# Kernel tuning notes

Hardware: AMD Instinct MI355X
Metric: run time of the kernel (lower is better)

## Reference

```python
import jax, jax.numpy as jnp
import numpy as np

N_NODES = 50000
N_EDGES = 1600000
IN_CH = 128
HID_CH = 128


def setup_inputs() -> dict:
    key = jax.random.key(0)
    ks = jax.random.split(key, 8)
    node_embed = jax.random.normal(ks[0], (N_NODES, IN_CH), dtype=jnp.float32)
    node_pos = jax.random.normal(ks[1], (N_NODES, 3), dtype=jnp.float32)
    edge_index = jax.random.randint(ks[2], (2, N_EDGES), 0, N_NODES, dtype=jnp.int64)
    # Linear weights stored as [in, out] so y = x @ W + b (matches torch x @ W.T + b)
    W_res = jax.random.normal(ks[3], (IN_CH, HID_CH), dtype=jnp.float32) / np.sqrt(IN_CH)
    W_msg = jax.random.normal(ks[4], (2 * IN_CH + 1, HID_CH), dtype=jnp.float32) / np.sqrt(2 * IN_CH + 1)
    b_msg = jax.random.normal(ks[5], (HID_CH,), dtype=jnp.float32) * 0.01
    W_upd = jax.random.normal(ks[6], (IN_CH + HID_CH, HID_CH), dtype=jnp.float32) / np.sqrt(IN_CH + HID_CH)
    b_upd = jax.random.normal(ks[7], (HID_CH,), dtype=jnp.float32) * 0.01
    return {"node_embed": node_embed, "node_pos": node_pos, "edge_index": edge_index,
            "W_res": W_res, "W_msg": W_msg, "b_msg": b_msg, "W_upd": W_upd, "b_upd": b_upd}


def reference(node_embed, node_pos, edge_index, W_res, W_msg, b_msg, W_upd, b_upd):
    row, col = edge_index[0], edge_index[1]
    # squared distance per edge: [E, 1]
    diff = node_pos[row] - node_pos[col]
    dist = jnp.sum(diff * diff, axis=1, keepdims=True)
    # message MLP on concat(src, tgt, dist): [E, 2*in+1] -> [E, hidden]
    msg_in = jnp.concatenate([node_embed[row], node_embed[col], dist], axis=-1)
    msg = jax.nn.relu(msg_in @ W_msg + b_msg)
    # scatter-sum messages into target nodes (index = col, as in original)
    aggr = jax.ops.segment_sum(msg, col, num_segments=N_NODES)
    upd_in = jnp.concatenate([node_embed, aggr], axis=-1)
    new_node_embed = node_embed @ W_res + jax.nn.relu(upd_in @ W_upd + b_upd)
    return new_node_embed
```

## Files before the change

### kernel.cpp

```cpp
#include <hip/hip_runtime.h>
#include <hip/hip_bf16.h>
#include <cstdint>


typedef __bf16 bf16x8 __attribute__((ext_vector_type(8)));
typedef float floatx4 __attribute__((ext_vector_type(4)));
typedef float floatx2 __attribute__((ext_vector_type(2)));
typedef unsigned int uintx4 __attribute__((ext_vector_type(4)));

#define BUCKET_CAP 128
#define NBINS 256
#define BIN_CAP 10240
#define PASS2_SPLIT 4
#define CUR_STRIDE 32

__device__ __forceinline__ ushort f2bf(float f) {
  union { float f; uint i; } v; v.f = f;
  uint r = v.i + 0x7fff + ((v.i >> 16) & 1);
  return (ushort)(r >> 16);
}
__device__ __forceinline__ bf16x8 load_frag(const ushort* p) {
  uint4 v = *(const uint4*)p;
  return __builtin_bit_cast(bf16x8, v);
}
__device__ __forceinline__ floatx2 pmax0(floatx2 a) {
#if __has_builtin(__builtin_elementwise_max)
  return __builtin_elementwise_max(a, (floatx2)(0.f));
#else
  floatx2 r; r.x = fmaxf(a.x, 0.f); r.y = fmaxf(a.y, 0.f); return r;
#endif
}
__device__ __forceinline__ floatx2 cvtpk2(uint qu) {
#if __has_builtin(__builtin_amdgcn_cvt_pk_f32_fp8)
  return __builtin_amdgcn_cvt_pk_f32_fp8((int)qu, false);
#else
  floatx2 o = {__builtin_amdgcn_cvt_f32_fp8((int)qu, 0),
               __builtin_amdgcn_cvt_f32_fp8((int)qu, 1)};
  return o;
#endif
}

struct WSrc { const float* s[5]; };

__global__ __launch_bounds__(256) void k01_cast_bin(
    const float* __restrict__ embed, ushort* __restrict__ Eb, int n4, int nb_cast,
    WSrc ws, ushort* __restrict__ Wt,
    const int* __restrict__ ei, int E,
    uint* __restrict__ bin_cursor, uint* __restrict__ binned, int bb)
{
  __shared__ uint hist[NBINS];
  __shared__ uint sbase[NBINS];
  __shared__ uint lcur[NBINS];

  if ((int)blockIdx.x >= bb) {
    int cb = blockIdx.x - bb;
    if (cb < nb_cast) {
      int i = cb * 256 + threadIdx.x;
      if (i < n4) {
        float4 v = ((const float4*)embed)[i];
        ushort4 o;
        o.x = f2bf(v.x); o.y = f2bf(v.y); o.z = f2bf(v.z); o.w = f2bf(v.w);
        ((ushort4*)Eb)[i] = o;
      }
      return;
    }
    int wb = cb - nb_cast;
    const float* s = ws.s[wb];
    ushort* d = Wt + wb * 16384;
    for (int i = threadIdx.x; i < 16384; i += 256) {
      int k = i >> 7, n = i & 127;
      d[n * 128 + k] = f2bf(s[i]);
    }
    return;
  }

  const int t = threadIdx.x;
  hist[t] = 0;
  __syncthreads();

  const int e0 = blockIdx.x * 2048 + t * 8;
  int rr[8], cc[8];
  bool any = (e0 < E);
  if (any) {
    int4 r0 = ((const int4*)(ei + e0))[0];
    int4 r1 = ((const int4*)(ei + e0))[1];
    int4 c0 = ((const int4*)(ei + E + e0))[0];
    int4 c1 = ((const int4*)(ei + E + e0))[1];
    rr[0]=r0.x; rr[1]=r0.y; rr[2]=r0.z; rr[3]=r0.w;
    rr[4]=r1.x; rr[5]=r1.y; rr[6]=r1.z; rr[7]=r1.w;
    cc[0]=c0.x; cc[1]=c0.y; cc[2]=c0.z; cc[3]=c0.w;
    cc[4]=c1.x; cc[5]=c1.y; cc[6]=c1.z; cc[7]=c1.w;
#pragma unroll
    for (int j = 0; j < 8; ++j) {
      if (e0 + j < E) atomicAdd(&hist[cc[j] >> 8], 1u);
    }
  }
  __syncthreads();
  uint h = hist[t];
  sbase[t] = h ? atomicAdd(bin_cursor + t * CUR_STRIDE, h) : 0u;
  lcur[t] = 0;
  __syncthreads();
  if (any) {
#pragma unroll
    for (int j = 0; j < 8; ++j) {
      if (e0 + j < E) {
        int b = cc[j] >> 8;
        uint ofs = atomicAdd(&lcur[b], 1u);
        uint idx = sbase[b] + ofs;
        if (idx < BIN_CAP)
          binned[(size_t)b * BIN_CAP + idx] = ((uint)cc[j] << 16) | (uint)rr[j];
      }
    }
  }
}

__global__ __launch_bounds__(256) void k2_proj_pass2(
    const ushort* __restrict__ Ab, int M, int rt,
    const ushort* __restrict__ W1t, const ushort* __restrict__ W2t,
    const float* __restrict__ b_msg, const float* __restrict__ pos,
    unsigned char* __restrict__ P1, ushort* __restrict__ P2b,
    const uint* __restrict__ bin_cursor, const uint* __restrict__ binned,
    int* __restrict__ counts, uint* __restrict__ recs)
{
  if ((int)blockIdx.x >= rt) {
    int b = blockIdx.x - rt;
    int bin = b / PASS2_SPLIT, part = b % PASS2_SPLIT;
    int cnt = (int)min(bin_cursor[bin * CUR_STRIDE], (uint)BIN_CAP);
    int s0 = (int)((long)cnt * part / PASS2_SPLIT);
    int s1 = (int)((long)cnt * (part + 1) / PASS2_SPLIT);
    const uint* src = binned + (size_t)bin * BIN_CAP;

    int i = s0 + threadIdx.x;
    for (; i + 768 < s1; i += 1024) {
      uint rc[4];
      rc[0] = src[i]; rc[1] = src[i + 256]; rc[2] = src[i + 512]; rc[3] = src[i + 768];
      float d[4];
#pragma unroll
      for (int j = 0; j < 4; ++j) {
        uint r = rc[j] & 0xffffu, c = rc[j] >> 16;
        float dx = pos[3 * r + 0] - pos[3 * c + 0];
        float dy = pos[3 * r + 1] - pos[3 * c + 1];
        float dz = pos[3 * r + 2] - pos[3 * c + 2];
        d[j] = dx * dx + dy * dy + dz * dz;
      }
#pragma unroll
      for (int j = 0; j < 4; ++j) {
        uint c = rc[j] >> 16;
        int slot = atomicAdd(counts + c, 1);
        if (slot < BUCKET_CAP)
          recs[(size_t)c * BUCKET_CAP + slot] = (rc[j] << 16) | (uint)f2bf(d[j]);
      }
    }
    for (; i < s1; i += 256) {
      uint rc = src[i];
      uint r = rc & 0xffffu, c = rc >> 16;
      float dx = pos[3 * r + 0] - pos[3 * c + 0];
      float dy = pos[3 * r + 1] - pos[3 * c + 1];
      float dz = pos[3 * r + 2] - pos[3 * c + 2];
      float dist = dx * dx + dy * dy + dz * dz;
      int slot = atomicAdd(counts + c, 1);
      if (slot < BUCKET_CAP)
        recs[(size_t)c * BUCKET_CAP + slot] = (rc << 16) | (uint)f2bf(dist);
    }
    return;
  }

  const int wv = threadIdx.x >> 6, lane = threadIdx.x & 63;
  const int q = lane >> 4, lr = lane & 15;
  const int m0 = blockIdx.x * 32;
  const int n0 = wv * 32;

  const ushort* Wt2[2] = {W1t, W2t};
  bf16x8 bfr[2][2][4];
#pragma unroll
  for (int ws = 0; ws < 2; ++ws)
#pragma unroll
    for (int nt = 0; nt < 2; ++nt) {
      int colc = n0 + nt * 16 + lr;
#pragma unroll
      for (int kc = 0; kc < 4; ++kc)
        bfr[ws][nt][kc] = load_frag(Wt2[ws] + colc * 128 + kc * 32 + q * 8);
    }

  floatx4 z = {0.f, 0.f, 0.f, 0.f};
  floatx4 acc[2][2][2];
#pragma unroll
  for (int ws = 0; ws < 2; ++ws)
#pragma unroll
    for (int mt = 0; mt < 2; ++mt)
#pragma unroll
      for (int nt = 0; nt < 2; ++nt) acc[ws][mt][nt] = z;

  const int r0 = min(m0 + lr, M - 1);
  const int r1 = min(m0 + 16 + lr, M - 1);
#pragma unroll
  for (int kc = 0; kc < 4; ++kc) {
    bf16x8 a0 = load_frag(Ab + (size_t)r0 * 128 + kc * 32 + q * 8);
    bf16x8 a1 = load_frag(Ab + (size_t)r1 * 128 + kc * 32 + q * 8);
#pragma unroll
    for (int ws = 0; ws < 2; ++ws)
#pragma unroll
      for (int nt = 0; nt < 2; ++nt) {
        acc[ws][0][nt] = __builtin_amdgcn_mfma_f32_16x16x32_bf16(a0, bfr[ws][nt][kc], acc[ws][0][nt], 0, 0, 0);
        acc[ws][1][nt] = __builtin_amdgcn_mfma_f32_16x16x32_bf16(a1, bfr[ws][nt][kc], acc[ws][1][nt], 0, 0, 0);
      }
  }

#pragma unroll
  for (int nt = 0; nt < 2; ++nt) {
    int colc = n0 + nt * 16 + lr;
    float bias = b_msg[colc];
#pragma unroll
    for (int mt = 0; mt < 2; ++mt)
#pragma unroll
      for (int i = 0; i < 4; ++i) {
        int r = m0 + mt * 16 + q * 4 + i;
        if (r < M) {
          int p8 = __builtin_amdgcn_cvt_pk_fp8_f32(acc[0][mt][nt][i], 0.f, 0, false);
          P1[(size_t)r * 128 + colc] = (unsigned char)(p8 & 0xff);
          P2b[(size_t)r * 128 + colc] = f2bf(acc[1][mt][nt][i] + bias);
        }
      }
  }
}

__global__ __launch_bounds__(256) void aggregate(const int* __restrict__ counts,
                                                 const uint* __restrict__ recs,
                                                 const unsigned char* __restrict__ P1,
                                                 const ushort* __restrict__ P2b,
                                                 const float* __restrict__ wd,
                                                 ushort* __restrict__ aggr, int M)
{
  const int lane = threadIdx.x & 63;
  const int ch = lane * 2;
  const int wid = blockIdx.x * 4 + (threadIdx.x >> 6);
  const int nw = gridDim.x * 4;

  float2 wl = *(const float2*)(wd + ch);
  floatx2 wv = {wl.x, wl.y};

  for (int n = wid; n < M; n += nw) {
    uint p2u = *(const uint*)(P2b + (size_t)n * 128 + ch);
    floatx2 p2 = {__int_as_float((int)(p2u << 16)),
                  __int_as_float((int)(p2u & 0xffff0000u))};

    const int cnt = min(counts[n], BUCKET_CAP);
    const uint* base = recs + (size_t)n * BUCKET_CAP;

    floatx2 accA = {0.f, 0.f}, accB = {0.f, 0.f};

    auto edge = [&](uint rec, floatx2& acc) {
      float d = __int_as_float((int)(rec << 16));
      uint off = ((rec >> 9) & 0x007fff80u) | (uint)ch;
      uint qu = (uint)*(const ushort*)(P1 + off);
#if __has_builtin(__builtin_elementwise_fma)
      floatx2 u = __builtin_elementwise_fma((floatx2)(d), wv, p2);
#else
      floatx2 u = (floatx2)(d) * wv + p2;
#endif
      floatx2 t = cvtpk2(qu) + u;
      acc += pmax0(t);
    };

    int i = 0;
    for (; i + 8 <= cnt; i += 8) {
      uintx4 ra = __builtin_nontemporal_load((const uintx4*)(base + i));
      uintx4 rb = __builtin_nontemporal_load((const uintx4*)(base + i + 4));
      edge(ra.x, accA); edge(ra.y, accB); edge(ra.z, accA); edge(ra.w, accB);
      edge(rb.x, accA); edge(rb.y, accB); edge(rb.z, accA); edge(rb.w, accB);
    }
    for (; i < cnt; ++i) edge(base[i], accA);

    floatx2 acc = accA + accB;
    uint o = (uint)f2bf(acc.x) | ((uint)f2bf(acc.y) << 16);
    *(uint*)(aggr + (size_t)n * 128 + ch) = o;
  }
}

__global__ __launch_bounds__(256) void gemm_upd_mfma(
    const ushort* __restrict__ Eb, const ushort* __restrict__ Gb, int M,
    const ushort* __restrict__ Wu1t, const ushort* __restrict__ Wu2t,
    const ushort* __restrict__ Wrt, const float* __restrict__ b_upd,
    float* __restrict__ out)
{
  const int wv = threadIdx.x >> 6, lane = threadIdx.x & 63;
  const int q = lane >> 4, lr = lane & 15;
  const int m0 = blockIdx.x * 32;
  const int n0 = wv * 32;

  bf16x8 b1[2][4], b2[2][4], br[2][4];
#pragma unroll
  for (int nt = 0; nt < 2; ++nt) {
    int colc = n0 + nt * 16 + lr;
#pragma unroll
    for (int kc = 0; kc < 4; ++kc) {
      b1[nt][kc] = load_frag(Wu1t + colc * 128 + kc * 32 + q * 8);
      b2[nt][kc] = load_frag(Wu2t + colc * 128 + kc * 32 + q * 8);
      br[nt][kc] = load_frag(Wrt  + colc * 128 + kc * 32 + q * 8);
    }
  }

  floatx4 z = {0.f, 0.f, 0.f, 0.f};
  floatx4 acc_u[2][2], acc_r[2][2];
#pragma unroll
  for (int mt = 0; mt < 2; ++mt)
#pragma unroll
    for (int nt = 0; nt < 2; ++nt) { acc_u[mt][nt] = z; acc_r[mt][nt] = z; }

  const int r0 = min(m0 + lr, M - 1);
  const int r1 = min(m0 + 16 + lr, M - 1);
#pragma unroll
  for (int kc = 0; kc < 4; ++kc) {
    bf16x8 ae0 = load_frag(Eb + (size_t)r0 * 128 + kc * 32 + q * 8);
    bf16x8 ae1 = load_frag(Eb + (size_t)r1 * 128 + kc * 32 + q * 8);
    bf16x8 ag0 = load_frag(Gb + (size_t)r0 * 128 + kc * 32 + q * 8);
    bf16x8 ag1 = load_frag(Gb + (size_t)r1 * 128 + kc * 32 + q * 8);
#pragma unroll
    for (int nt = 0; nt < 2; ++nt) {
      acc_u[0][nt] = __builtin_amdgcn_mfma_f32_16x16x32_bf16(ae0, b1[nt][kc], acc_u[0][nt], 0, 0, 0);
      acc_u[1][nt] = __builtin_amdgcn_mfma_f32_16x16x32_bf16(ae1, b1[nt][kc], acc_u[1][nt], 0, 0, 0);
      acc_u[0][nt] = __builtin_amdgcn_mfma_f32_16x16x32_bf16(ag0, b2[nt][kc], acc_u[0][nt], 0, 0, 0);
      acc_u[1][nt] = __builtin_amdgcn_mfma_f32_16x16x32_bf16(ag1, b2[nt][kc], acc_u[1][nt], 0, 0, 0);
      acc_r[0][nt] = __builtin_amdgcn_mfma_f32_16x16x32_bf16(ae0, br[nt][kc], acc_r[0][nt], 0, 0, 0);
      acc_r[1][nt] = __builtin_amdgcn_mfma_f32_16x16x32_bf16(ae1, br[nt][kc], acc_r[1][nt], 0, 0, 0);
    }
  }

#pragma unroll
  for (int nt = 0; nt < 2; ++nt) {
    int colc = n0 + nt * 16 + lr;
    float bias = b_upd[colc];
#pragma unroll
    for (int mt = 0; mt < 2; ++mt)
#pragma unroll
      for (int i = 0; i < 4; ++i) {
        int r = m0 + mt * 16 + q * 4 + i;
        if (r < M)
          out[(size_t)r * 128 + colc] = acc_r[mt][nt][i] + fmaxf(acc_u[mt][nt][i] + bias, 0.f);
      }
  }
}

extern "C" void kernel_launch(void* const* d_in, const int* in_sizes, int n_in,
                              void* d_out, int out_size, void* d_ws, size_t ws_size,
                              hipStream_t stream)
{
  const float* embed = (const float*)d_in[0];
  const float* pos   = (const float*)d_in[1];
  const int*   ei    = (const int*)d_in[2];
  const float* W_res = (const float*)d_in[3];
  const float* W_msg = (const float*)d_in[4];
  const float* b_msg = (const float*)d_in[5];
  const float* W_upd = (const float*)d_in[6];
  const float* b_upd = (const float*)d_in[7];
  float* out = (float*)d_out;

  const int M = in_sizes[0] / 128;
  const int E = in_sizes[2] / 2;

  ushort* Eb = (ushort*)d_ws;
  unsigned char* P1f8 = (unsigned char*)(Eb + (size_t)M * 128);
  ushort* P2b = (ushort*)(P1f8 + (size_t)M * 128);
  ushort* Gb  = P2b + (size_t)M * 128;
  ushort* Wt  = Gb  + (size_t)M * 128;
  uint*   recs = (uint*)(Wt + 5 * 16384);
  uint*   binned = (uint*)(recs + (size_t)M * BUCKET_CAP);
  int*    counts = (int*)(binned + (size_t)NBINS * BIN_CAP);
  uint*   bin_cursor = (uint*)(counts + M);

  (void)hipMemsetAsync(counts, 0, (size_t)(M + NBINS * CUR_STRIDE) * sizeof(int), stream);

  WSrc wsrc;
  wsrc.s[0] = W_msg;
  wsrc.s[1] = W_msg + 128 * 128;
  wsrc.s[2] = W_res;
  wsrc.s[3] = W_upd;
  wsrc.s[4] = W_upd + 128 * 128;

  int n4 = M * 128 / 4;
  int nb_cast = (n4 + 255) / 256;
  int bb = (E + 2047) / 2048;
  k01_cast_bin<<<bb + nb_cast + 5, 256, 0, stream>>>(
      embed, Eb, n4, nb_cast, wsrc, Wt, ei, E, bin_cursor, binned, bb);

  int rt = (M + 31) / 32;
  k2_proj_pass2<<<rt + NBINS * PASS2_SPLIT, 256, 0, stream>>>(
      Eb, M, rt, Wt, Wt + 16384, b_msg, pos, P1f8, P2b,
      bin_cursor, binned, counts, recs);

  int ab = min((M + 3) / 4, 2048);
  aggregate<<<ab, 256, 0, stream>>>(counts, recs, P1f8, P2b,
                                    W_msg + 256 * 128, Gb, M);

  gemm_upd_mfma<<<rt, 256, 0, stream>>>(Eb, Gb, M, Wt + 3 * 16384, Wt + 4 * 16384,
                                        Wt + 2 * 16384, b_upd, out);
}
```

Before: 276.8 us.

## Replace per-node atomic buckets with per-bin shared-memory counting sort

Bins edges by target node into 1024 bins of 64 columns, then each second-pass block does a local counting sort in shared memory, writing compact CSR-like sorted records with per-node start and count. This removes the global per-node atomic slot allocation, the fixed 128-slot buckets, and the large counts memset, and improves locality of the aggregate reads. The cost is more shared memory per block (which affects the GEMM blocks in the same kernel too) and hard bin capacity limits that could drop edges for skewed inputs.

```diff
diff --git a/kernel.cpp b/kernel.cpp
--- a/kernel.cpp
+++ b/kernel.cpp
@@ -8,10 +8,9 @@
 typedef float floatx2 __attribute__((ext_vector_type(2)));
 typedef unsigned int uintx4 __attribute__((ext_vector_type(4)));
 
-#define BUCKET_CAP 128
-#define NBINS 256
-#define BIN_CAP 10240
-#define PASS2_SPLIT 4
+#define NBINS 1024
+#define BIN_CAP 2560
+#define CAP_OUT 2816
 #define CUR_STRIDE 32
 
 __device__ __forceinline__ ushort f2bf(float f) {
@@ -75,7 +74,8 @@
   }
 
   const int t = threadIdx.x;
-  hist[t] = 0;
+#pragma unroll
+  for (int k = 0; k < NBINS / 256; ++k) hist[t + k * 256] = 0;
   __syncthreads();
 
   const int e0 = blockIdx.x * 2048 + t * 8;
@@ -92,19 +92,23 @@
     cc[4]=c1.x; cc[5]=c1.y; cc[6]=c1.z; cc[7]=c1.w;
 #pragma unroll
     for (int j = 0; j < 8; ++j) {
-      if (e0 + j < E) atomicAdd(&hist[cc[j] >> 8], 1u);
+      if (e0 + j < E) atomicAdd(&hist[cc[j] >> 6], 1u);
     }
   }
   __syncthreads();
-  uint h = hist[t];
-  sbase[t] = h ? atomicAdd(bin_cursor + t * CUR_STRIDE, h) : 0u;
-  lcur[t] = 0;
+#pragma unroll
+  for (int k = 0; k < NBINS / 256; ++k) {
+    int b2 = t + k * 256;
+    uint h = hist[b2];
+    sbase[b2] = h ? atomicAdd(bin_cursor + b2 * CUR_STRIDE, h) : 0u;
+    lcur[b2] = 0;
+  }
   __syncthreads();
   if (any) {
 #pragma unroll
     for (int j = 0; j < 8; ++j) {
       if (e0 + j < E) {
-        int b = cc[j] >> 8;
+        int b = cc[j] >> 6;
         uint ofs = atomicAdd(&lcur[b], 1u);
         uint idx = sbase[b] + ofs;
         if (idx < BIN_CAP)
@@ -114,53 +118,64 @@
   }
 }
 
-__global__ __launch_bounds__(256) void k2_proj_pass2(
+__global__ __launch_bounds__(256) void k2_proj_sort(
     const ushort* __restrict__ Ab, int M, int rt,
     const ushort* __restrict__ W1t, const ushort* __restrict__ W2t,
     const float* __restrict__ b_msg, const float* __restrict__ pos,
     unsigned char* __restrict__ P1, ushort* __restrict__ P2b,
     const uint* __restrict__ bin_cursor, const uint* __restrict__ binned,
-    int* __restrict__ counts, uint* __restrict__ recs)
+    uint* __restrict__ sorted, int* __restrict__ nstart, int* __restrict__ ncnt)
 {
+  __shared__ ushort sdist[BIN_CAP];
+  __shared__ uint   srt[CAP_OUT];
+  __shared__ float  spos[64 * 3];
+  __shared__ uint   h[64], st[64], lc[64];
+  __shared__ uint   stot;
+
   if ((int)blockIdx.x >= rt) {
-    int b = blockIdx.x - rt;
-    int bin = b / PASS2_SPLIT, part = b % PASS2_SPLIT;
-    int cnt = (int)min(bin_cursor[bin * CUR_STRIDE], (uint)BIN_CAP);
-    int s0 = (int)((long)cnt * part / PASS2_SPLIT);
-    int s1 = (int)((long)cnt * (part + 1) / PASS2_SPLIT);
+    const int bin = blockIdx.x - rt;
+    const int col0 = bin * 64;
+    const int tid = threadIdx.x;
+    const int cnt = (int)min(bin_cursor[bin * CUR_STRIDE], (uint)BIN_CAP);
     const uint* src = binned + (size_t)bin * BIN_CAP;
-
-    int i = s0 + threadIdx.x;
-    for (; i + 768 < s1; i += 1024) {
-      uint rc[4];
-      rc[0] = src[i]; rc[1] = src[i + 256]; rc[2] = src[i + 512]; rc[3] = src[i + 768];
-      float d[4];
-#pragma unroll
-      for (int j = 0; j < 4; ++j) {
-        uint r = rc[j] & 0xffffu, c = rc[j] >> 16;
-        float dx = pos[3 * r + 0] - pos[3 * c + 0];
-        float dy = pos[3 * r + 1] - pos[3 * c + 1];
-        float dz = pos[3 * r + 2] - pos[3 * c + 2];
-        d[j] = dx * dx + dy * dy + dz * dz;
-      }
-#pragma unroll
-      for (int j = 0; j < 4; ++j) {
-        uint c = rc[j] >> 16;
-        int slot = atomicAdd(counts + c, 1);
-        if (slot < BUCKET_CAP)
-          recs[(size_t)c * BUCKET_CAP + slot] = (rc[j] << 16) | (uint)f2bf(d[j]);
-      }
-    }
-    for (; i < s1; i += 256) {
+    const int ncol = min(64, M - col0);
+
+    if (tid < 64) { h[tid] = 0; lc[tid] = 0; }
+    for (int i = tid; i < ncol * 3; i += 256) spos[i] = pos[(size_t)col0 * 3 + i];
+    __syncthreads();
+
+    for (int i = tid; i < cnt; i += 256) {
       uint rc = src[i];
-      uint r = rc & 0xffffu, c = rc >> 16;
-      float dx = pos[3 * r + 0] - pos[3 * c + 0];
-      float dy = pos[3 * r + 1] - pos[3 * c + 1];
-      float dz = pos[3 * r + 2] - pos[3 * c + 2];
-      float dist = dx * dx + dy * dy + dz * dz;
-      int slot = atomicAdd(counts + c, 1);
-      if (slot < BUCKET_CAP)
-        recs[(size_t)c * BUCKET_CAP + slot] = (rc << 16) | (uint)f2bf(dist);
+      uint row = rc & 0xffffu, cl = (rc >> 16) & 63u;
+      float dx = spos[cl * 3 + 0] - pos[(size_t)row * 3 + 0];
+      float dy = spos[cl * 3 + 1] - pos[(size_t)row * 3 + 1];
+      float dz = spos[cl * 3 + 2] - pos[(size_t)row * 3 + 2];
+      sdist[i] = f2bf(dx * dx + dy * dy + dz * dz);
+      atomicAdd(&h[cl], 1u);
+    }
+    __syncthreads();
+
+    if (tid == 0) {
+      uint s = 0;
+      for (int c = 0; c < 64; ++c) { st[c] = s; s += (h[c] + 3u) & ~3u; }
+      stot = s;
+    }
+    __syncthreads();
+
+    for (int i = tid; i < cnt; i += 256) {
+      uint rc = src[i];
+      uint row = rc & 0xffffu, cl = (rc >> 16) & 63u;
+      uint p = st[cl] + atomicAdd(&lc[cl], 1u);
+      if (p < CAP_OUT) srt[p] = (row << 16) | (uint)sdist[i];
+    }
+    __syncthreads();
+
+    uint tot = min(stot, (uint)CAP_OUT);
+    for (int i = tid; i < (int)tot; i += 256)
+      sorted[(size_t)bin * CAP_OUT + i] = srt[i];
+    if (tid < 64 && tid < ncol) {
+      nstart[col0 + tid] = bin * CAP_OUT + (int)st[tid];
+      ncnt[col0 + tid] = (int)h[tid];
     }
     return;
   }
@@ -224,8 +239,9 @@
   }
 }
 
-__global__ __launch_bounds__(256) void aggregate(const int* __restrict__ counts,
-                                                 const uint* __restrict__ recs,
+__global__ __launch_bounds__(256) void aggregate(const int* __restrict__ ncnt,
+                                                 const int* __restrict__ nstart,
+                                                 const uint* __restrict__ sorted,
                                                  const unsigned char* __restrict__ P1,
                                                  const ushort* __restrict__ P2b,
                                                  const float* __restrict__ wd,
@@ -244,8 +260,8 @@
     floatx2 p2 = {__int_as_float((int)(p2u << 16)),
                   __int_as_float((int)(p2u & 0xffff0000u))};
 
-    const int cnt = min(counts[n], BUCKET_CAP);
-    const uint* base = recs + (size_t)n * BUCKET_CAP;
+    const int cnt = ncnt[n];
+    const uint* base = sorted + nstart[n];
 
     floatx2 accA = {0.f, 0.f}, accB = {0.f, 0.f};
 
@@ -363,12 +379,13 @@
   ushort* P2b = (ushort*)(P1f8 + (size_t)M * 128);
   ushort* Gb  = P2b + (size_t)M * 128;
   ushort* Wt  = Gb  + (size_t)M * 128;
-  uint*   recs = (uint*)(Wt + 5 * 16384);
-  uint*   binned = (uint*)(recs + (size_t)M * BUCKET_CAP);
-  int*    counts = (int*)(binned + (size_t)NBINS * BIN_CAP);
-  uint*   bin_cursor = (uint*)(counts + M);
-
-  (void)hipMemsetAsync(counts, 0, (size_t)(M + NBINS * CUR_STRIDE) * sizeof(int), stream);
+  uint*   binned = (uint*)(Wt + 5 * 16384);
+  uint*   sorted = binned + (size_t)NBINS * BIN_CAP;
+  int*    nstart = (int*)(sorted + (size_t)NBINS * CAP_OUT);
+  int*    ncnt   = nstart + M;
+  uint*   bin_cursor = (uint*)(ncnt + M);
+
+  (void)hipMemsetAsync(bin_cursor, 0, (size_t)NBINS * CUR_STRIDE * sizeof(uint), stream);
 
   WSrc wsrc;
   wsrc.s[0] = W_msg;
@@ -384,12 +401,13 @@
       embed, Eb, n4, nb_cast, wsrc, Wt, ei, E, bin_cursor, binned, bb);
 
   int rt = (M + 31) / 32;
-  k2_proj_pass2<<<rt + NBINS * PASS2_SPLIT, 256, 0, stream>>>(
+  int nbin2 = (M + 63) / 64;
+  k2_proj_sort<<<rt + nbin2, 256, 0, stream>>>(
       Eb, M, rt, Wt, Wt + 16384, b_msg, pos, P1f8, P2b,
-      bin_cursor, binned, counts, recs);
+      bin_cursor, binned, sorted, nstart, ncnt);
 
   int ab = min((M + 3) / 4, 2048);
-  aggregate<<<ab, 256, 0, stream>>>(counts, recs, P1f8, P2b,
+  aggregate<<<ab, 256, 0, stream>>>(ncnt, nstart, sorted, P1f8, P2b,
                                     W_msg + 256 * 128, Gb, M);
 
   gemm_upd_mfma<<<rt, 256, 0, stream>>>(Eb, Gb, M, Wt + 3 * 16384, Wt + 4 * 16384,
```

Result: faster. 271.4 us (-2.0%).
